# Performance work log

Hardware: AMD Instinct MI355X
Metric: run time of the kernel (lower is better)

Reference implementation:

```python
import jax, jax.numpy as jnp
import numpy as np

N = 100000          # nodes
E = 1600000         # edges
F_IN = 128          # in_channels
C = 32              # hidden_channels (per head)
H = 4               # heads
NEG_SLOPE = 0.2     # PyG GATConv default leaky_relu slope


def setup_inputs() -> dict:
    key = jax.random.key(0)
    ks = jax.random.split(key, 6)
    x = jax.random.normal(ks[0], (N, F_IN), dtype=jnp.float32)
    edge_index = jax.random.randint(ks[1], (2, E), 0, N, dtype=jnp.int32)
    # learned params (PyG GATConv: lin weight, att_src, att_dst, bias)
    W = jax.random.normal(ks[2], (F_IN, H * C), dtype=jnp.float32) * (1.0 / np.sqrt(F_IN))
    att_src = jax.random.normal(ks[3], (H, C), dtype=jnp.float32) * 0.1
    att_dst = jax.random.normal(ks[4], (H, C), dtype=jnp.float32) * 0.1
    bias = jnp.zeros((H * C,), dtype=jnp.float32)
    return {"x": x, "edge_index": edge_index, "W": W,
            "att_src": att_src, "att_dst": att_dst, "bias": bias}


def reference(x, edge_index, W, att_src, att_dst, bias):
    # linear projection, split into heads: [N, H, C]
    h = (x @ W).reshape(N, H, C)
    # per-node attention terms: [N, H]
    a_src = jnp.einsum('nhc,hc->nh', h, att_src)
    a_dst = jnp.einsum('nhc,hc->nh', h, att_dst)
    src, dst = edge_index[0], edge_index[1]
    # edge-wise logits: [E, H]
    alpha = jax.nn.leaky_relu(a_src[src] + a_dst[dst], NEG_SLOPE)
    # segment softmax over incoming edges of each dst node
    amax = jax.ops.segment_max(alpha, dst, num_segments=N)       # [N, H]
    amax = jnp.where(jnp.isfinite(amax), amax, 0.0)
    ex = jnp.exp(alpha - amax[dst])                              # [E, H]
    denom = jax.ops.segment_sum(ex, dst, num_segments=N)         # [N, H]
    alpha = ex / (denom[dst] + 1e-16)                            # [E, H]
    # weighted messages, scatter-add to dst: [N, H, C]
    msg = h[src] * alpha[:, :, None]
    out = jax.ops.segment_sum(msg, dst, num_segments=N)
    out = out.reshape(N, H * C) + bias
    return jax.nn.elu(out)
```

## Files before the change

kernel.cpp:

```cpp
#include <hip/hip_runtime.h>
#include <hip/hip_bf16.h>
#include <math.h>

#define N_NODES 100000
#define N_EDGES 1600000
#define NEG_SLOPE 0.2f

#define NB_BUCKET 782
#define ST_CAP 2560

#define OFF_H     0
#define OFF_ASRC  25600000
#define OFF_ADST  27200000
#define OFF_OFFS  28800000
#define OFF_BCNT  29200128
#define OFF_BOFF  29204224
#define OFF_BCUR  29208320
#define OFF_TMP   29212416
#define OFF_CSR   35612416

__device__ __forceinline__ float leaky(float x) {
    return fmaxf(x, NEG_SLOPE * x);
}
__device__ __forceinline__ float sel4(int h, float a, float b, float c, float d) {
    return h == 0 ? a : (h == 1 ? b : (h == 2 ? c : d));
}
__device__ __forceinline__ float2 bf2_to_f2(unsigned int u) {
    float2 r;
    r.x = __uint_as_float(u << 16);
    r.y = __uint_as_float(u & 0xffff0000u);
    return r;
}
__device__ __forceinline__ void wave_lds_fence() {
    asm volatile("s_waitcnt lgkmcnt(0)" ::: "memory");
    __builtin_amdgcn_sched_barrier(0);
}

#define BR 64
#define KT 32
__global__ __launch_bounds__(256, 4) void gemm_att_kernel(
    const float* __restrict__ x, const float* __restrict__ W,
    const float* __restrict__ att_src, const float* __restrict__ att_dst,
    __hip_bfloat162* __restrict__ h_bf, float* __restrict__ a_src,
    float* __restrict__ a_dst)
{
    __shared__ float xs[KT][68];
    __shared__ float ws[KT][132];

    const int tid = threadIdx.x;
    const int cx  = tid & 31;
    const int ry  = tid >> 5;
    const int n0  = blockIdx.x * BR;

    float acc[8][4];
#pragma unroll
    for (int i = 0; i < 8; ++i)
#pragma unroll
        for (int j = 0; j < 4; ++j) acc[i][j] = 0.f;

    const int sr  = tid >> 3;
    const int skk = (tid & 7) * 4;
    const int wc4 = (tid & 31) * 4;
    const int wk  = tid >> 5;

    for (int k0 = 0; k0 < 128; k0 += KT) {
#pragma unroll
        for (int rr = 0; rr < BR; rr += 32) {
            int row = n0 + sr + rr;
            row = row < N_NODES ? row : N_NODES - 1;
            const float4 v = *(const float4*)&x[(size_t)row * 128 + k0 + skk];
            xs[skk + 0][sr + rr] = v.x;
            xs[skk + 1][sr + rr] = v.y;
            xs[skk + 2][sr + rr] = v.z;
            xs[skk + 3][sr + rr] = v.w;
        }
#pragma unroll
        for (int kk2 = 0; kk2 < KT; kk2 += 8) {
            const float4 wv = *(const float4*)&W[(size_t)(k0 + wk + kk2) * 128 + wc4];
            *(float4*)&ws[wk + kk2][wc4] = wv;
        }
        __syncthreads();

#pragma unroll 4
        for (int k = 0; k < KT; ++k) {
            const float4 wv = *(const float4*)&ws[k][cx * 4];
            const float4 xa = *(const float4*)&xs[k][ry * 8];
            const float4 xb = *(const float4*)&xs[k][ry * 8 + 4];
            const float xr[8] = {xa.x, xa.y, xa.z, xa.w, xb.x, xb.y, xb.z, xb.w};
            const float wr[4] = {wv.x, wv.y, wv.z, wv.w};
#pragma unroll
            for (int i = 0; i < 8; ++i)
#pragma unroll
                for (int j = 0; j < 4; ++j)
                    acc[i][j] = fmaf(xr[i], wr[j], acc[i][j]);
        }
        __syncthreads();
    }

    const float4 as4 = ((const float4*)att_src)[cx];
    const float4 ad4 = ((const float4*)att_dst)[cx];
    const int hd = cx >> 3;

#pragma unroll
    for (int i = 0; i < 8; ++i) {
        const int row = n0 + ry * 8 + i;
        if (row >= N_NODES) break;
        union { __hip_bfloat162 h2[2]; uint2 u2; } pk;
        pk.h2[0].x = __float2bfloat16(acc[i][0]);
        pk.h2[0].y = __float2bfloat16(acc[i][1]);
        pk.h2[1].x = __float2bfloat16(acc[i][2]);
        pk.h2[1].y = __float2bfloat16(acc[i][3]);
        ((uint2*)h_bf)[(size_t)row * 32 + cx] = pk.u2;

        float vs = acc[i][0] * as4.x + acc[i][1] * as4.y + acc[i][2] * as4.z + acc[i][3] * as4.w;
        float vd = acc[i][0] * ad4.x + acc[i][1] * ad4.y + acc[i][2] * ad4.z + acc[i][3] * ad4.w;
#pragma unroll
        for (int off = 1; off < 8; off <<= 1) {
            vs += __shfl_xor(vs, off);
            vd += __shfl_xor(vd, off);
        }
        if ((cx & 7) == 0) {
            a_src[row * 4 + hd] = vs;
            a_dst[row * 4 + hd] = vd;
        }
    }
}

#define BH_EPB 6250
__global__ __launch_bounds__(256) void bucket_hist_kernel(
    const int* __restrict__ dst, int* __restrict__ bcnt)
{
    __shared__ int cnt[NB_BUCKET];
    const int tid = threadIdx.x;
    for (int i = tid; i < NB_BUCKET; i += 256) cnt[i] = 0;
    __syncthreads();
    const int e0 = blockIdx.x * BH_EPB;
    for (int i = tid; i < BH_EPB; i += 256)
        atomicAdd(&cnt[dst[e0 + i] >> 7], 1);
    __syncthreads();
    for (int i = tid; i < NB_BUCKET; i += 256)
        if (cnt[i]) atomicAdd(&bcnt[i], cnt[i]);
}

__global__ __launch_bounds__(1024) void bucket_scan_kernel(
    const int* __restrict__ bcnt, int* __restrict__ boff, int* __restrict__ bcur)
{
    const int tid  = threadIdx.x;
    const int lane = tid & 63;
    const int wv   = tid >> 6;
    const int v    = (tid < NB_BUCKET) ? bcnt[tid] : 0;

    int sv = v;
#pragma unroll
    for (int off = 1; off < 64; off <<= 1) {
        int u = __shfl_up(sv, off);
        if (lane >= off) sv += u;
    }
    __shared__ int wsum[16];
    if (lane == 63) wsum[wv] = sv;
    __syncthreads();
    if (tid == 0) {
        int run = 0;
#pragma unroll
        for (int k = 0; k < 16; ++k) { int t = wsum[k]; wsum[k] = run; run += t; }
    }
    __syncthreads();
    if (tid < NB_BUCKET) {
        const int excl = wsum[wv] + sv - v;
        boff[tid] = excl;
        bcur[tid] = excl;
    }
    if (tid == 0) boff[NB_BUCKET] = N_EDGES;
}

#define S1_EPB 6250
__global__ __launch_bounds__(256) void scat1_kernel(
    const int* __restrict__ src, const int* __restrict__ dst,
    int* __restrict__ bcur, unsigned int* __restrict__ tmp)
{
    __shared__ int cnt[NB_BUCKET];
    const int tid = threadIdx.x;
    for (int i = tid; i < NB_BUCKET; i += 256) cnt[i] = 0;
    __syncthreads();
    const int e0 = blockIdx.x * S1_EPB;
    for (int i = tid; i < S1_EPB; i += 256)
        atomicAdd(&cnt[dst[e0 + i] >> 7], 1);
    __syncthreads();
    for (int b = tid; b < NB_BUCKET; b += 256) {
        const int c = cnt[b];
        cnt[b] = c ? atomicAdd(&bcur[b], c) : 0;
    }
    __syncthreads();
    for (int i = tid; i < S1_EPB; i += 256) {
        const int d = dst[e0 + i];
        const int s = src[e0 + i];
        const int p = atomicAdd(&cnt[d >> 7], 1);
        tmp[p] = ((unsigned int)s << 7) | (unsigned int)(d & 127);
    }
}

__global__ __launch_bounds__(256) void phaseB_kernel(
    const unsigned int* __restrict__ tmp, const int* __restrict__ boff,
    int* __restrict__ offs, int* __restrict__ csr)
{
    __shared__ unsigned int st[ST_CAP];
    __shared__ int hist[128];
    __shared__ int cur[128];
    __shared__ int wtot[4];

    const int b    = blockIdx.x;
    const int tid  = threadIdx.x;
    const int lane = tid & 63;
    const int wv   = tid >> 6;
    const int base = boff[b];
    const int cnt  = boff[b + 1] - base;

    if (tid < 128) hist[tid] = 0;
    __syncthreads();

    for (int i = tid; i < cnt; i += 256) {
        const unsigned int v = tmp[base + i];
        if (i < ST_CAP) st[i] = v;
        atomicAdd(&hist[v & 127], 1);
    }
    __syncthreads();

    const int hv = (tid < 128) ? hist[tid] : 0;
    int sv = hv;
#pragma unroll
    for (int off = 1; off < 64; off <<= 1) {
        int u = __shfl_up(sv, off);
        if (lane >= off) sv += u;
    }
    if (lane == 63) wtot[wv] = sv;
    __syncthreads();
    const int wpre = (wv > 0 ? wtot[0] : 0) + (wv > 1 ? wtot[1] : 0) + (wv > 2 ? wtot[2] : 0);
    if (tid < 128) {
        const int excl = wpre + sv - hv;
        cur[tid] = excl;
        const int node = (b << 7) + tid;
        if (node < N_NODES) offs[node] = base + excl;
    }
    if (b == 0 && tid == 0) offs[N_NODES] = N_EDGES;
    __syncthreads();

    for (int i = tid; i < cnt; i += 256) {
        const unsigned int v = (i < ST_CAP) ? st[i] : tmp[base + i];
        const int p = atomicAdd(&cur[v & 127], 1);
        csr[base + p] = (int)(v >> 7);
    }
}

__global__ __launch_bounds__(256, 4) void gat_agg_kernel(
    const int* __restrict__ csr_src, const int* __restrict__ offs,
    const __hip_bfloat162* __restrict__ h_bf,
    const float* __restrict__ a_src, const float* __restrict__ a_dst,
    const float* __restrict__ bias, float* __restrict__ out)
{
    __shared__ float4 stage[4][128];

    const int wv   = threadIdx.x >> 6;
    const int lane = threadIdx.x & 63;
    const int node = blockIdx.x * 4 + wv;

    const int start = offs[node];
    const int deg   = offs[node + 1] - start;

    const float4 ad4 = ((const float4*)a_dst)[node];

    float sf = __int_as_float(0);
    float e0 = 0.f, e1 = 0.f, e2 = 0.f, e3 = 0.f;
    if (lane < deg) {
        const int s = csr_src[start + lane];
        sf = __int_as_float(s);
        const float4 as4 = ((const float4*)a_src)[s];
        e0 = __expf(leaky(as4.x + ad4.x));
        e1 = __expf(leaky(as4.y + ad4.y));
        e2 = __expf(leaky(as4.z + ad4.z));
        e3 = __expf(leaky(as4.w + ad4.w));
    }
    stage[wv][lane * 2 + 0] = make_float4(sf, e0, sf, e1);
    stage[wv][lane * 2 + 1] = make_float4(sf, e2, sf, e3);
    wave_lds_fence();

    if (deg <= 64) {
        const int qw   = lane >> 4;
        const int cpos = lane & 15;
        const int hsub = cpos >> 2;
        const float2* sp = (const float2*)&stage[wv][0];
        const uint4*  hp = (const uint4*)h_bf;

        float acc[8];
#pragma unroll
        for (int i = 0; i < 8; ++i) acc[i] = 0.f;
        float den = 0.f;

        for (int j = 0; j < deg; j += 16) {
#pragma unroll
            for (int u = 0; u < 4; ++u) {
                const float2 se = sp[(j + u * 4 + qw) * 4 + hsub];
                const float ev = se.y;
                const unsigned s = (unsigned)__float_as_int(se.x);
                const uint4 hv = hp[(size_t)(s * 16u + (unsigned)cpos)];
                float2 f;
                f = bf2_to_f2(hv.x);
                acc[0] = fmaf(ev, f.x, acc[0]);
                acc[1] = fmaf(ev, f.y, acc[1]);
                f = bf2_to_f2(hv.y);
                acc[2] = fmaf(ev, f.x, acc[2]);
                acc[3] = fmaf(ev, f.y, acc[3]);
                f = bf2_to_f2(hv.z);
                acc[4] = fmaf(ev, f.x, acc[4]);
                acc[5] = fmaf(ev, f.y, acc[5]);
                f = bf2_to_f2(hv.w);
                acc[6] = fmaf(ev, f.x, acc[6]);
                acc[7] = fmaf(ev, f.y, acc[7]);
                den += ev;
            }
        }

#pragma unroll
        for (int i = 0; i < 8; ++i) acc[i] += __shfl_xor(acc[i], 16);
#pragma unroll
        for (int i = 0; i < 8; ++i) acc[i] += __shfl_xor(acc[i], 32);
        den += __shfl_xor(den, 16);
        den += __shfl_xor(den, 32);

        const float inv = 1.0f / (den + 1e-16f);
#pragma unroll
        for (int i = 0; i < 8; ++i) acc[i] *= inv;

        if (qw == 0) {
            float4* sf4 = (float4*)&stage[wv][0];
            sf4[cpos * 2 + 0] = make_float4(acc[0], acc[1], acc[2], acc[3]);
            sf4[cpos * 2 + 1] = make_float4(acc[4], acc[5], acc[6], acc[7]);
        }
        wave_lds_fence();
        const float2 v  = ((const float2*)&stage[wv][0])[lane];
        const float2 b2 = ((const float2*)bias)[lane];
        float ox = v.x + b2.x;
        float oy = v.y + b2.y;
        ox = ox > 0.f ? ox : __expf(ox) - 1.f;
        oy = oy > 0.f ? oy : __expf(oy) - 1.f;
        ((float2*)out)[(size_t)node * 64 + lane] = make_float2(ox, oy);
    } else {
        const int hidx = lane >> 4;
        const float adh = sel4(hidx, ad4.x, ad4.y, ad4.z, ad4.w);
        float2 acc = {0.f, 0.f};
        float  den = 0.f;
        for (int j = 0; j < deg; ++j) {
            const int s = csr_src[start + j];
            const float ash = a_src[s * 4 + hidx];
            const float ex = __expf(leaky(ash + adh));
            const float2 f = __bfloat1622float2(h_bf[(size_t)s * 64 + lane]);
            acc.x += ex * f.x;
            acc.y += ex * f.y;
            den   += ex;
        }
        const float inv = 1.0f / (den + 1e-16f);
        const float2 b2 = ((const float2*)bias)[lane];
        float ox = acc.x * inv + b2.x;
        float oy = acc.y * inv + b2.y;
        ox = ox > 0.f ? ox : expm1f(ox);
        oy = oy > 0.f ? oy : expm1f(oy);
        ((float2*)out)[(size_t)node * 64 + lane] = make_float2(ox, oy);
    }
}

extern "C" void kernel_launch(void* const* d_in, const int* in_sizes, int n_in,
                              void* d_out, int out_size, void* d_ws, size_t ws_size,
                              hipStream_t stream)
{
    const float* x       = (const float*)d_in[0];
    const int*   ei      = (const int*)  d_in[1];
    const float* W       = (const float*)d_in[2];
    const float* att_src = (const float*)d_in[3];
    const float* att_dst = (const float*)d_in[4];
    const float* bias    = (const float*)d_in[5];
    float*       out     = (float*)d_out;

    char* ws = (char*)d_ws;
    __hip_bfloat162* h_bf = (__hip_bfloat162*)(ws + OFF_H);
    float* a_src = (float*)(ws + OFF_ASRC);
    float* a_dst = (float*)(ws + OFF_ADST);
    int*   offs  = (int*)  (ws + OFF_OFFS);
    int*   bcnt  = (int*)  (ws + OFF_BCNT);
    int*   boff  = (int*)  (ws + OFF_BOFF);
    int*   bcur  = (int*)  (ws + OFF_BCUR);
    unsigned int* tmp = (unsigned int*)(ws + OFF_TMP);
    int*   csr   = (int*)  (ws + OFF_CSR);

    const int* srcp = ei;
    const int* dstp = ei + N_EDGES;

    hipMemsetAsync(bcnt, 0, NB_BUCKET * sizeof(int), stream);

    gemm_att_kernel<<<(N_NODES + BR - 1) / BR, 256, 0, stream>>>(
        x, W, att_src, att_dst, h_bf, a_src, a_dst);

    bucket_hist_kernel<<<N_EDGES / BH_EPB, 256, 0, stream>>>(dstp, bcnt);
    bucket_scan_kernel<<<1, 1024, 0, stream>>>(bcnt, boff, bcur);
    scat1_kernel<<<N_EDGES / S1_EPB, 256, 0, stream>>>(srcp, dstp, bcur, tmp);
    phaseB_kernel<<<NB_BUCKET, 256, 0, stream>>>(tmp, boff, offs, csr);

    gat_agg_kernel<<<N_NODES / 4, 256, 0, stream>>>(
        csr, offs, h_bf, a_src, a_dst, bias, out);
}
```

Before: 280.5 us.

## Drop LDS staging in GAT aggregation; compute edge weights per lane inline

```diff
diff --git a/kernel.cpp b/kernel.cpp
--- a/kernel.cpp
+++ b/kernel.cpp
@@ -22,18 +22,11 @@
 __device__ __forceinline__ float leaky(float x) {
     return fmaxf(x, NEG_SLOPE * x);
 }
-__device__ __forceinline__ float sel4(int h, float a, float b, float c, float d) {
-    return h == 0 ? a : (h == 1 ? b : (h == 2 ? c : d));
-}
 __device__ __forceinline__ float2 bf2_to_f2(unsigned int u) {
     float2 r;
     r.x = __uint_as_float(u << 16);
     r.y = __uint_as_float(u & 0xffff0000u);
     return r;
-}
-__device__ __forceinline__ void wave_lds_fence() {
-    asm volatile("s_waitcnt lgkmcnt(0)" ::: "memory");
-    __builtin_amdgcn_sched_barrier(0);
 }
 
 #define BR 64
@@ -251,57 +244,39 @@
     }
 }
 
-__global__ __launch_bounds__(256, 4) void gat_agg_kernel(
+__global__ __launch_bounds__(256, 8) void gat_agg_kernel(
     const int* __restrict__ csr_src, const int* __restrict__ offs,
     const __hip_bfloat162* __restrict__ h_bf,
     const float* __restrict__ a_src, const float* __restrict__ a_dst,
     const float* __restrict__ bias, float* __restrict__ out)
 {
-    __shared__ float4 stage[4][128];
-
     const int wv   = threadIdx.x >> 6;
     const int lane = threadIdx.x & 63;
     const int node = blockIdx.x * 4 + wv;
+    const int qw   = lane >> 4;
+    const int cpos = lane & 15;
+    const int hsub = cpos >> 2;
 
     const int start = offs[node];
     const int deg   = offs[node + 1] - start;
 
-    const float4 ad4 = ((const float4*)a_dst)[node];
-
-    float sf = __int_as_float(0);
-    float e0 = 0.f, e1 = 0.f, e2 = 0.f, e3 = 0.f;
-    if (lane < deg) {
-        const int s = csr_src[start + lane];
-        sf = __int_as_float(s);
-        const float4 as4 = ((const float4*)a_src)[s];
-        e0 = __expf(leaky(as4.x + ad4.x));
-        e1 = __expf(leaky(as4.y + ad4.y));
-        e2 = __expf(leaky(as4.z + ad4.z));
-        e3 = __expf(leaky(as4.w + ad4.w));
-    }
-    stage[wv][lane * 2 + 0] = make_float4(sf, e0, sf, e1);
-    stage[wv][lane * 2 + 1] = make_float4(sf, e2, sf, e3);
-    wave_lds_fence();
-
-    if (deg <= 64) {
-        const int qw   = lane >> 4;
-        const int cpos = lane & 15;
-        const int hsub = cpos >> 2;
-        const float2* sp = (const float2*)&stage[wv][0];
-        const uint4*  hp = (const uint4*)h_bf;
-
-        float acc[8];
-#pragma unroll
-        for (int i = 0; i < 8; ++i) acc[i] = 0.f;
-        float den = 0.f;
-
-        for (int j = 0; j < deg; j += 16) {
-#pragma unroll
-            for (int u = 0; u < 4; ++u) {
-                const float2 se = sp[(j + u * 4 + qw) * 4 + hsub];
-                const float ev = se.y;
-                const unsigned s = (unsigned)__float_as_int(se.x);
-                const uint4 hv = hp[(size_t)(s * 16u + (unsigned)cpos)];
+    const float adh = a_dst[node * 4 + hsub];
+    const uint4* hp = (const uint4*)h_bf;
+
+    float acc[8];
+#pragma unroll
+    for (int i = 0; i < 8; ++i) acc[i] = 0.f;
+    float den = 0.f;
+
+    for (int e0 = qw; e0 < deg; e0 += 16) {
+#pragma unroll
+        for (int u = 0; u < 4; ++u) {
+            const int e = e0 + u * 4;
+            if (e < deg) {
+                const int s = csr_src[start + e];
+                const float ash = a_src[s * 4 + hsub];
+                const float ev = __expf(leaky(ash + adh));
+                const uint4 hv = hp[(size_t)s * 16 + cpos];
                 float2 f;
                 f = bf2_to_f2(hv.x);
                 acc[0] = fmaf(ev, f.x, acc[0]);
@@ -318,52 +293,31 @@
                 den += ev;
             }
         }
-
-#pragma unroll
-        for (int i = 0; i < 8; ++i) acc[i] += __shfl_xor(acc[i], 16);
-#pragma unroll
-        for (int i = 0; i < 8; ++i) acc[i] += __shfl_xor(acc[i], 32);
-        den += __shfl_xor(den, 16);
-        den += __shfl_xor(den, 32);
-
-        const float inv = 1.0f / (den + 1e-16f);
-#pragma unroll
-        for (int i = 0; i < 8; ++i) acc[i] *= inv;
-
-        if (qw == 0) {
-            float4* sf4 = (float4*)&stage[wv][0];
-            sf4[cpos * 2 + 0] = make_float4(acc[0], acc[1], acc[2], acc[3]);
-            sf4[cpos * 2 + 1] = make_float4(acc[4], acc[5], acc[6], acc[7]);
-        }
-        wave_lds_fence();
-        const float2 v  = ((const float2*)&stage[wv][0])[lane];
-        const float2 b2 = ((const float2*)bias)[lane];
-        float ox = v.x + b2.x;
-        float oy = v.y + b2.y;
+    }
+
+#pragma unroll
+    for (int i = 0; i < 8; ++i) {
+        acc[i] += __shfl_xor(acc[i], 16);
+        acc[i] += __shfl_xor(acc[i], 32);
+    }
+    den += __shfl_xor(den, 16);
+    den += __shfl_xor(den, 32);
+
+    const float inv = 1.0f / (den + 1e-16f);
+
+    if (qw < 2) {
+        const float4 b4 = ((const float4*)bias)[cpos * 2 + qw];
+        const int a0 = qw * 4;
+        float ox = acc[a0 + 0] * inv + b4.x;
+        float oy = acc[a0 + 1] * inv + b4.y;
+        float oz = acc[a0 + 2] * inv + b4.z;
+        float ow = acc[a0 + 3] * inv + b4.w;
         ox = ox > 0.f ? ox : __expf(ox) - 1.f;
         oy = oy > 0.f ? oy : __expf(oy) - 1.f;
-        ((float2*)out)[(size_t)node * 64 + lane] = make_float2(ox, oy);
-    } else {
-        const int hidx = lane >> 4;
-        const float adh = sel4(hidx, ad4.x, ad4.y, ad4.z, ad4.w);
-        float2 acc = {0.f, 0.f};
-        float  den = 0.f;
-        for (int j = 0; j < deg; ++j) {
-            const int s = csr_src[start + j];
-            const float ash = a_src[s * 4 + hidx];
-            const float ex = __expf(leaky(ash + adh));
-            const float2 f = __bfloat1622float2(h_bf[(size_t)s * 64 + lane]);
-            acc.x += ex * f.x;
-            acc.y += ex * f.y;
-            den   += ex;
-        }
-        const float inv = 1.0f / (den + 1e-16f);
-        const float2 b2 = ((const float2*)bias)[lane];
-        float ox = acc.x * inv + b2.x;
-        float oy = acc.y * inv + b2.y;
-        ox = ox > 0.f ? ox : expm1f(ox);
-        oy = oy > 0.f ? oy : expm1f(oy);
-        ((float2*)out)[(size_t)node * 64 + lane] = make_float2(ox, oy);
+        oz = oz > 0.f ? oz : __expf(oz) - 1.f;
+        ow = ow > 0.f ? ow : __expf(ow) - 1.f;
+        ((float4*)out)[(size_t)node * 32 + cpos * 2 + qw] =
+            make_float4(ox, oy, oz, ow);
     }
 }
 
```

Result: slower. 290.1 us (+3.5%).

## Replace FP32 SIMT projection GEMM with split-bf16 MFMA GEMM

Applied to the files above, without the earlier changes.

```diff
diff --git a/kernel.cpp b/kernel.cpp
--- a/kernel.cpp
+++ b/kernel.cpp
@@ -18,6 +18,12 @@
 #define OFF_BCUR  29208320
 #define OFF_TMP   29212416
 #define OFF_CSR   35612416
+#define OFF_WHT   42012416
+#define OFF_WLT   42045184
+
+typedef __attribute__((ext_vector_type(8))) __bf16 bf16x8;
+typedef __attribute__((ext_vector_type(4))) float  f32x4;
+union BF8 { unsigned u32[4]; bf16x8 v; };
 
 __device__ __forceinline__ float leaky(float x) {
     return fmaxf(x, NEG_SLOPE * x);
@@ -31,97 +37,135 @@
     r.y = __uint_as_float(u & 0xffff0000u);
     return r;
 }
+__device__ __forceinline__ unsigned bf16_rne(float f) {
+    const unsigned b = __float_as_uint(f);
+    return ((b + 0x7FFFu + ((b >> 16) & 1u)) >> 16) & 0xFFFFu;
+}
+__device__ __forceinline__ float bf16_tof(unsigned hb) {
+    return __uint_as_float(hb << 16);
+}
 __device__ __forceinline__ void wave_lds_fence() {
     asm volatile("s_waitcnt lgkmcnt(0)" ::: "memory");
     __builtin_amdgcn_sched_barrier(0);
 }
 
-#define BR 64
-#define KT 32
-__global__ __launch_bounds__(256, 4) void gemm_att_kernel(
-    const float* __restrict__ x, const float* __restrict__ W,
+__global__ __launch_bounds__(256) void wprep_kernel(
+    const float* __restrict__ W, ushort* __restrict__ WhT, ushort* __restrict__ WlT)
+{
+    const int idx = blockIdx.x * 256 + threadIdx.x;
+    const int n = idx >> 7, k = idx & 127;
+    const float w  = W[k * 128 + n];
+    const unsigned hb = bf16_rne(w);
+    const float rs = w - bf16_tof(hb);
+    const unsigned lb = bf16_rne(rs);
+    WhT[n * 128 + k] = (ushort)hb;
+    WlT[n * 128 + k] = (ushort)lb;
+}
+
+__global__ __launch_bounds__(256, 2) void gemm_mfma_kernel(
+    const float* __restrict__ x, const ushort* __restrict__ WhT,
+    const ushort* __restrict__ WlT,
     const float* __restrict__ att_src, const float* __restrict__ att_dst,
-    __hip_bfloat162* __restrict__ h_bf, float* __restrict__ a_src,
-    float* __restrict__ a_dst)
-{
-    __shared__ float xs[KT][68];
-    __shared__ float ws[KT][132];
-
-    const int tid = threadIdx.x;
-    const int cx  = tid & 31;
-    const int ry  = tid >> 5;
-    const int n0  = blockIdx.x * BR;
-
-    float acc[8][4];
-#pragma unroll
-    for (int i = 0; i < 8; ++i)
-#pragma unroll
-        for (int j = 0; j < 4; ++j) acc[i][j] = 0.f;
-
-    const int sr  = tid >> 3;
-    const int skk = (tid & 7) * 4;
-    const int wc4 = (tid & 31) * 4;
-    const int wk  = tid >> 5;
-
-    for (int k0 = 0; k0 < 128; k0 += KT) {
-#pragma unroll
-        for (int rr = 0; rr < BR; rr += 32) {
-            int row = n0 + sr + rr;
-            row = row < N_NODES ? row : N_NODES - 1;
-            const float4 v = *(const float4*)&x[(size_t)row * 128 + k0 + skk];
-            xs[skk + 0][sr + rr] = v.x;
-            xs[skk + 1][sr + rr] = v.y;
-            xs[skk + 2][sr + rr] = v.z;
-            xs[skk + 3][sr + rr] = v.w;
-        }
-#pragma unroll
-        for (int kk2 = 0; kk2 < KT; kk2 += 8) {
-            const float4 wv = *(const float4*)&W[(size_t)(k0 + wk + kk2) * 128 + wc4];
-            *(float4*)&ws[wk + kk2][wc4] = wv;
-        }
-        __syncthreads();
-
-#pragma unroll 4
-        for (int k = 0; k < KT; ++k) {
-            const float4 wv = *(const float4*)&ws[k][cx * 4];
-            const float4 xa = *(const float4*)&xs[k][ry * 8];
-            const float4 xb = *(const float4*)&xs[k][ry * 8 + 4];
-            const float xr[8] = {xa.x, xa.y, xa.z, xa.w, xb.x, xb.y, xb.z, xb.w};
-            const float wr[4] = {wv.x, wv.y, wv.z, wv.w};
-#pragma unroll
-            for (int i = 0; i < 8; ++i)
-#pragma unroll
-                for (int j = 0; j < 4; ++j)
-                    acc[i][j] = fmaf(xr[i], wr[j], acc[i][j]);
-        }
-        __syncthreads();
-    }
-
-    const float4 as4 = ((const float4*)att_src)[cx];
-    const float4 ad4 = ((const float4*)att_dst)[cx];
-    const int hd = cx >> 3;
-
-#pragma unroll
-    for (int i = 0; i < 8; ++i) {
-        const int row = n0 + ry * 8 + i;
-        if (row >= N_NODES) break;
-        union { __hip_bfloat162 h2[2]; uint2 u2; } pk;
-        pk.h2[0].x = __float2bfloat16(acc[i][0]);
-        pk.h2[0].y = __float2bfloat16(acc[i][1]);
-        pk.h2[1].x = __float2bfloat16(acc[i][2]);
-        pk.h2[1].y = __float2bfloat16(acc[i][3]);
-        ((uint2*)h_bf)[(size_t)row * 32 + cx] = pk.u2;
-
-        float vs = acc[i][0] * as4.x + acc[i][1] * as4.y + acc[i][2] * as4.z + acc[i][3] * as4.w;
-        float vd = acc[i][0] * ad4.x + acc[i][1] * ad4.y + acc[i][2] * ad4.z + acc[i][3] * ad4.w;
-#pragma unroll
-        for (int off = 1; off < 8; off <<= 1) {
-            vs += __shfl_xor(vs, off);
-            vd += __shfl_xor(vd, off);
-        }
-        if ((cx & 7) == 0) {
-            a_src[row * 4 + hd] = vs;
-            a_dst[row * 4 + hd] = vd;
+    ushort* __restrict__ h_u16, float* __restrict__ a_src, float* __restrict__ a_dst)
+{
+    const int wv   = threadIdx.x >> 6;
+    const int lane = threadIdx.x & 63;
+    const int c15  = lane & 15;
+    const int kg   = lane >> 4;
+    const int r0g  = blockIdx.x * 128 + wv * 32;
+
+    bf16x8 ah[2][4], al[2][4];
+#pragma unroll
+    for (int mt = 0; mt < 2; ++mt) {
+        int row = r0g + mt * 16 + c15;
+        row = row < N_NODES ? row : N_NODES - 1;
+        const float4* xp = (const float4*)&x[(size_t)row * 128];
+#pragma unroll
+        for (int ks = 0; ks < 4; ++ks) {
+            const int kb = ks * 32 + kg * 8;
+            const float4 fa = xp[kb >> 2];
+            const float4 fb = xp[(kb >> 2) + 1];
+            const float f[8] = {fa.x, fa.y, fa.z, fa.w, fb.x, fb.y, fb.z, fb.w};
+            BF8 H, L;
+#pragma unroll
+            for (int j = 0; j < 4; ++j) {
+                const unsigned h0 = bf16_rne(f[2 * j + 0]);
+                const unsigned h1 = bf16_rne(f[2 * j + 1]);
+                const unsigned l0 = bf16_rne(f[2 * j + 0] - bf16_tof(h0));
+                const unsigned l1 = bf16_rne(f[2 * j + 1] - bf16_tof(h1));
+                H.u32[j] = h0 | (h1 << 16);
+                L.u32[j] = l0 | (l1 << 16);
+            }
+            ah[mt][ks] = H.v;
+            al[mt][ks] = L.v;
+        }
+    }
+
+    f32x4 acc[2][8];
+#pragma unroll
+    for (int mt = 0; mt < 2; ++mt)
+#pragma unroll
+        for (int nt = 0; nt < 8; ++nt)
+            acc[mt][nt] = (f32x4){0.f, 0.f, 0.f, 0.f};
+
+#pragma unroll
+    for (int ks = 0; ks < 4; ++ks) {
+        const int kb = ks * 32 + kg * 8;
+#pragma unroll
+        for (int nt = 0; nt < 8; ++nt) {
+            const int col = nt * 16 + c15;
+            const bf16x8 bh = *(const bf16x8*)&WhT[col * 128 + kb];
+            const bf16x8 bl = *(const bf16x8*)&WlT[col * 128 + kb];
+            acc[0][nt] = __builtin_amdgcn_mfma_f32_16x16x32_bf16(ah[0][ks], bh, acc[0][nt], 0, 0, 0);
+            acc[1][nt] = __builtin_amdgcn_mfma_f32_16x16x32_bf16(ah[1][ks], bh, acc[1][nt], 0, 0, 0);
+            acc[0][nt] = __builtin_amdgcn_mfma_f32_16x16x32_bf16(al[0][ks], bh, acc[0][nt], 0, 0, 0);
+            acc[1][nt] = __builtin_amdgcn_mfma_f32_16x16x32_bf16(al[1][ks], bh, acc[1][nt], 0, 0, 0);
+            acc[0][nt] = __builtin_amdgcn_mfma_f32_16x16x32_bf16(ah[0][ks], bl, acc[0][nt], 0, 0, 0);
+            acc[1][nt] = __builtin_amdgcn_mfma_f32_16x16x32_bf16(ah[1][ks], bl, acc[1][nt], 0, 0, 0);
+        }
+    }
+
+    float asv[8], adv[8];
+#pragma unroll
+    for (int nt = 0; nt < 8; ++nt) {
+        asv[nt] = att_src[nt * 16 + c15];
+        adv[nt] = att_dst[nt * 16 + c15];
+    }
+#pragma unroll
+    for (int mt = 0; mt < 2; ++mt) {
+#pragma unroll
+        for (int reg = 0; reg < 4; ++reg) {
+            const int row = r0g + mt * 16 + kg * 4 + reg;
+            const bool ok = row < N_NODES;
+            if (ok) {
+#pragma unroll
+                for (int nt = 0; nt < 8; ++nt)
+                    h_u16[(size_t)row * 128 + nt * 16 + c15] =
+                        (ushort)bf16_rne(acc[mt][nt][reg]);
+            }
+            float ps[4], pd[4];
+#pragma unroll
+            for (int hh = 0; hh < 4; ++hh) {
+                ps[hh] = acc[mt][2 * hh][reg] * asv[2 * hh] +
+                         acc[mt][2 * hh + 1][reg] * asv[2 * hh + 1];
+                pd[hh] = acc[mt][2 * hh][reg] * adv[2 * hh] +
+                         acc[mt][2 * hh + 1][reg] * adv[2 * hh + 1];
+            }
+#pragma unroll
+            for (int off = 1; off < 16; off <<= 1) {
+#pragma unroll
+                for (int hh = 0; hh < 4; ++hh) {
+                    ps[hh] += __shfl_xor(ps[hh], off);
+                    pd[hh] += __shfl_xor(pd[hh], off);
+                }
+            }
+            if (ok && c15 == 0) {
+#pragma unroll
+                for (int hh = 0; hh < 4; ++hh) {
+                    a_src[row * 4 + hh] = ps[hh];
+                    a_dst[row * 4 + hh] = pd[hh];
+                }
+            }
         }
     }
 }
@@ -380,6 +424,7 @@
     float*       out     = (float*)d_out;
 
     char* ws = (char*)d_ws;
+    ushort* h_u16 = (ushort*)(ws + OFF_H);
     __hip_bfloat162* h_bf = (__hip_bfloat162*)(ws + OFF_H);
     float* a_src = (float*)(ws + OFF_ASRC);
     float* a_dst = (float*)(ws + OFF_ADST);
@@ -389,14 +434,18 @@
     int*   bcur  = (int*)  (ws + OFF_BCUR);
     unsigned int* tmp = (unsigned int*)(ws + OFF_TMP);
     int*   csr   = (int*)  (ws + OFF_CSR);
+    ushort* WhT  = (ushort*)(ws + OFF_WHT);
+    ushort* WlT  = (ushort*)(ws + OFF_WLT);
 
     const int* srcp = ei;
     const int* dstp = ei + N_EDGES;
 
     hipMemsetAsync(bcnt, 0, NB_BUCKET * sizeof(int), stream);
 
-    gemm_att_kernel<<<(N_NODES + BR - 1) / BR, 256, 0, stream>>>(
-        x, W, att_src, att_dst, h_bf, a_src, a_dst);
+    wprep_kernel<<<64, 256, 0, stream>>>(W, WhT, WlT);
+
+    gemm_mfma_kernel<<<(N_NODES + 127) / 128, 256, 0, stream>>>(
+        x, WhT, WlT, att_src, att_dst, h_u16, a_src, a_dst);
 
     bucket_hist_kernel<<<N_EDGES / BH_EPB, 256, 0, stream>>>(dstp, bcnt);
     bucket_scan_kernel<<<1, 1024, 0, stream>>>(bcnt, boff, bcur);
```

After: 281.3 us. About the same (+0.3%).
